# Kernel optimization log

Hardware: AMD Instinct MI355X
Metric: run time of the kernel (lower is better)

## Reference

```python
import jax, jax.numpy as jnp
import numpy as np

B, H, D, DV, N, M = 1, 8, 64, 64, 2048, 128


def setup_inputs() -> dict:
    key = jax.random.key(0)
    k1, k2, k3, k4 = jax.random.split(key, 4)
    keys = jax.random.normal(k1, (B, H, D, N), dtype=jnp.float32)
    values = jax.random.normal(k2, (B, H, DV, N), dtype=jnp.float32)
    queries = jax.random.normal(k3, (B, H, D, N), dtype=jnp.float32)
    # orthonormal random features: QR of (m, key_dim) gaussian (reduced QR, m >= key_dim)
    raw = np.asarray(jax.random.normal(k4, (M, D), dtype=jnp.float32), dtype=np.float64)
    features = jnp.asarray(np.linalg.qr(raw)[0], dtype=jnp.float32)  # (M, D)
    return {"keys": keys, "values": values, "queries": queries, "features": features}


def reference(keys, values, queries, features):
    b, h, d, n = keys.shape
    dv = values.shape[2]
    m = features.shape[0]
    phi_scale = 1.0 / jnp.sqrt(jnp.asarray(m, keys.dtype))
    # flatten heads into batch, move locations to axis 1: (B*H, N, D)
    k = keys.reshape(b * h, d, n).transpose(0, 2, 1)
    v = values.reshape(b * h, dv, n).transpose(0, 2, 1)
    q = queries.reshape(b * h, d, n).transpose(0, 2, 1)

    def phi(x):  # (BH, N, D) -> (BH, N, M); f=[relu], h(x)=1.0
        return jax.nn.relu(jnp.einsum('bnd,md->bnm', x, features)) * phi_scale

    phi_k = phi(k)
    phi_q = phi(q)
    # causal linear attention: prefix sums of phi_k (x) v outer products
    kv = jnp.cumsum(phi_k[:, :, :, None] * v[:, :, None, :], axis=1)  # (BH, N, M, DV)
    out = jnp.einsum('bnm,bnmv->bnv', phi_q, kv)                      # (BH, N, DV)
    norm = jnp.einsum('bnm,bnm->bn', phi_q, jnp.cumsum(phi_k, axis=1))
    out = out / norm[:, :, None]
    out = out.transpose(0, 2, 1).reshape(b, h, dv, n)
    return out
```

## Files before the change

### kernel.cpp

```cpp
#include <hip/hip_runtime.h>


#define BH 8
#define D 64
#define DV 64
#define NSEQ 2048
#define M 128
#define CHK 64
#define NC (NSEQ / CHK)
#define PHI_SCALE 0.08838834764831845f

typedef unsigned int uint;
typedef unsigned short ushort;
typedef __attribute__((ext_vector_type(8))) short bf16x8;
typedef __attribute__((ext_vector_type(4))) short bf16x4;
typedef __attribute__((ext_vector_type(4))) float f32x4;
#define MFMA16(a, b, c) __builtin_amdgcn_mfma_f32_16x16x32_bf16((a), (b), (c), 0, 0, 0)

__device__ __forceinline__ short f2bf(float x) {
    uint u = __float_as_uint(x);
    u += 0x7fffu + ((u >> 16) & 1u);
    return (short)(u >> 16);
}
__device__ __forceinline__ float bf2f(short b) {
    return __uint_as_float(((uint)(ushort)b) << 16);
}

#define SWZ64(r, c)  ((r) * 64  + ((c) ^ (((r) & 7) << 3)))
#define SWZ128(r, c) ((r) * 128 + ((c) ^ (((r) & 7) << 3)))

__global__ __launch_bounds__(256) void favor_p1(
    const float* __restrict__ keys, const float* __restrict__ values,
    const float* __restrict__ queries, const float* __restrict__ features,
    ushort* __restrict__ St, float* __restrict__ z,
    ushort* __restrict__ pQg, ushort* __restrict__ pKg)
{
    const int bh = blockIdx.x >> 5, c = blockIdx.x & 31, n0 = c * CHK;
    const int tid = threadIdx.x;
    const int lane = tid & 63, wid = tid >> 6, quad = lane >> 4, l16 = lane & 15;

    __shared__ ulong2 smv[4096];
    short* sF    = (short*)smv;
    short* sPKmn = (short*)smv + 8192;
    short* sPQt  = (short*)smv + 16384;
    short* sPKt  = (short*)smv + 24576;

    const float* Kb = keys    + bh * D * NSEQ + n0 + 16 * wid + l16;
    const float* Qb = queries + bh * D * NSEQ + n0 + 16 * wid + l16;
    bf16x8 bK[2], aQ[2], aV[2];
    for (int h = 0; h < 2; ++h)
        for (int j = 0; j < 8; ++j) {
            const int d = 32 * h + 8 * quad + j;
            bK[h][j] = f2bf(Kb[d * NSEQ]);
            aQ[h][j] = f2bf(Qb[d * NSEQ]);
        }
    {
        const float* Vb = values + bh * DV * NSEQ + n0;
        for (int h = 0; h < 2; ++h) {
            const float4* vp = (const float4*)(Vb + (16 * wid + l16) * NSEQ + 32 * h + 8 * quad);
            float4 v0 = vp[0], v1 = vp[1];
            aV[h][0] = f2bf(v0.x); aV[h][1] = f2bf(v0.y);
            aV[h][2] = f2bf(v0.z); aV[h][3] = f2bf(v0.w);
            aV[h][4] = f2bf(v1.x); aV[h][5] = f2bf(v1.y);
            aV[h][6] = f2bf(v1.z); aV[h][7] = f2bf(v1.w);
        }
    }
    for (int k = 0; k < 8; ++k) {
        const int i = tid + 256 * k;
        float4 f = ((const float4*)features)[i];
        const int e = 4 * i, row = e >> 6, col = e & 63;
        bf16x4 bq;
        bq[0] = f2bf(f.x); bq[1] = f2bf(f.y); bq[2] = f2bf(f.z); bq[3] = f2bf(f.w);
        *(bf16x4*)(sF + SWZ64(row, col)) = bq;
    }
    __syncthreads();

    for (int mt = 0; mt < 8; ++mt) {
        f32x4 aMN = {0.f,0.f,0.f,0.f}, aQm = {0.f,0.f,0.f,0.f}, aKm = {0.f,0.f,0.f,0.f};
        for (int h = 0; h < 2; ++h) {
            bf16x8 fF = *(const bf16x8*)(sF + SWZ64(16 * mt + l16, 32 * h + 8 * quad));
            aMN = MFMA16(fF, bK[h], aMN);
            aQm = MFMA16(aQ[h], fF, aQm);
            aKm = MFMA16(bK[h], fF, aKm);
        }
        for (int r = 0; r < 4; ++r) {
            const int mr = 16 * mt + 4 * quad + r;
            sPKmn[SWZ64(mr, 16 * wid + l16)] = f2bf(fmaxf(aMN[r], 0.f) * PHI_SCALE);
            const int nr = 16 * wid + 4 * quad + r;
            sPQt[SWZ128(nr, 16 * mt + l16)] = f2bf(fmaxf(aQm[r], 0.f) * PHI_SCALE);
            sPKt[SWZ128(nr, 16 * mt + l16)] = f2bf(fmaxf(aKm[r], 0.f) * PHI_SCALE);
        }
    }
    __syncthreads();

    if (tid < 128) {
        float s = 0.f;
        for (int k = 0; k < 8; ++k) {
            bf16x8 v8 = *(const bf16x8*)(sPKmn + SWZ64(tid, 8 * k));
            for (int j = 0; j < 8; ++j) s += bf2f(v8[j]);
        }
        z[(bh * NC + c) * M + tid] = s;
    }

    {
        ushort* So = St + (size_t)(bh * NC + c) * (DV * M);
        for (int mt = 0; mt < 8; ++mt) {
            f32x4 acc = {0.f,0.f,0.f,0.f};
            for (int h = 0; h < 2; ++h) {
                bf16x8 bP = *(const bf16x8*)(sPKmn + SWZ64(16 * mt + l16, 32 * h + 8 * quad));
                acc = MFMA16(aV[h], bP, acc);
            }
            for (int r = 0; r < 4; ++r)
                So[(16 * wid + 4 * quad + r) * M + 16 * mt + l16] = (ushort)f2bf(acc[r]);
        }
    }

    {
        ushort* pQc = pQg + (size_t)(bh * NC + c) * 8192;
        ushort* pKc = pKg + (size_t)(bh * NC + c) * 8192;
        const ulong2* sq = (const ulong2*)sPQt;
        const ulong2* sk = (const ulong2*)sPKt;
        for (int i = tid; i < 1024; i += 256) {
            ((ulong2*)pQc)[i] = sq[i];
            ((ulong2*)pKc)[i] = sk[i];
        }
    }
}

__global__ __launch_bounds__(256) void favor_p2k(
    const float* __restrict__ values, const ushort* __restrict__ St,
    const float* __restrict__ z, const ushort* __restrict__ pQg,
    const ushort* __restrict__ pKg, float* __restrict__ out)
{
    const int bh = blockIdx.x >> 5, c = blockIdx.x & 31, n0 = c * CHK;
    const int tid = threadIdx.x;
    const int lane = tid & 63, wid = tid >> 6, quad = lane >> 4, l16 = lane & 15;

    __shared__ ulong2 smv[4144];
    short* sPQt = (short*)smv;
    short* sPKt = (short*)smv + 8192;
    short* sSx  = (short*)smv + 16384;
    short* sV   = (short*)smv + 24576;
    short* sAm  = (short*)smv + 28672;
    float* sNm  = (float*)((char*)smv + 65536);
    float* sZ   = (float*)((char*)smv + 65792);
    float* sOut = (float*)((char*)smv + 32768);

    {
        const ulong2* pQc = (const ulong2*)(pQg + (size_t)(bh * NC + c) * 8192);
        const ulong2* pKc = (const ulong2*)(pKg + (size_t)(bh * NC + c) * 8192);
        ulong2* dq = (ulong2*)sPQt;
        ulong2* dk = (ulong2*)sPKt;
        for (int i = tid; i < 1024; i += 256) {
            dq[i] = pQc[i];
            dk[i] = pKc[i];
        }
    }

    {
        const int v = tid >> 2, cb = (tid & 3) * 16;
        const float4* vp = (const float4*)(values + (bh * DV + v) * NSEQ + n0 + cb);
        float4 f0 = vp[0], f1 = vp[1], f2 = vp[2], f3 = vp[3];
        bf16x8 lo, hi;
        lo[0] = f2bf(f0.x); lo[1] = f2bf(f0.y); lo[2] = f2bf(f0.z); lo[3] = f2bf(f0.w);
        lo[4] = f2bf(f1.x); lo[5] = f2bf(f1.y); lo[6] = f2bf(f1.z); lo[7] = f2bf(f1.w);
        hi[0] = f2bf(f2.x); hi[1] = f2bf(f2.y); hi[2] = f2bf(f2.z); hi[3] = f2bf(f2.w);
        hi[4] = f2bf(f3.x); hi[5] = f2bf(f3.y); hi[6] = f2bf(f3.z); hi[7] = f2bf(f3.w);
        *(bf16x8*)(sV + SWZ64(v, cb))     = lo;
        *(bf16x8*)(sV + SWZ64(v, cb + 8)) = hi;
    }

    if (tid < 128) {
        float s = 0.f;
        const float* zp = z + bh * NC * M + tid;
        #pragma unroll 4
        for (int cc = 0; cc < c; ++cc) s += zp[cc * M];
        sZ[tid] = s;
    }

    {
        float a32[4][8];
        #pragma unroll
        for (int k = 0; k < 4; ++k)
            #pragma unroll
            for (int j = 0; j < 8; ++j) a32[k][j] = 0.f;
        const ushort* Sb = St + (size_t)bh * NC * 8192;
        for (int cc = 0; cc < c; ++cc) {
            const ushort* p = Sb + (size_t)cc * 8192;
            #pragma unroll
            for (int k = 0; k < 4; ++k) {
                bf16x8 v8 = *(const bf16x8*)(p + 8 * (tid + 256 * k));
                #pragma unroll
                for (int j = 0; j < 8; ++j) a32[k][j] += bf2f(v8[j]);
            }
        }
        #pragma unroll
        for (int k = 0; k < 4; ++k) {
            const int e = tid + 256 * k;
            bf16x8 w;
            #pragma unroll
            for (int j = 0; j < 8; ++j) w[j] = f2bf(a32[k][j]);
            *(bf16x8*)(sSx + SWZ128(e >> 4, 8 * (e & 15))) = w;
        }
    }
    __syncthreads();

    f32x4 accO[4], accC[4];
    for (int t = 0; t < 4; ++t) { accO[t] = (f32x4){0.f,0.f,0.f,0.f}; accC[t] = (f32x4){0.f,0.f,0.f,0.f}; }
    for (int mt = 0; mt < 4; ++mt) {
        bf16x8 aP = *(const bf16x8*)(sPQt + SWZ128(16 * wid + l16, 32 * mt + 8 * quad));
        for (int jt = 0; jt < 4; ++jt) {
            bf16x8 bK2 = *(const bf16x8*)(sPKt + SWZ128(16 * jt + l16, 32 * mt + 8 * quad));
            accC[jt] = MFMA16(aP, bK2, accC[jt]);
        }
    }
    float rsum[4] = {0.f, 0.f, 0.f, 0.f};
    for (int jt = 0; jt < 4; ++jt)
        for (int r = 0; r < 4; ++r) {
            const int n = 16 * wid + 4 * quad + r;
            const int j = 16 * jt + l16;
            const float av = (j <= n) ? accC[jt][r] : 0.f;
            rsum[r] += av;
            sAm[SWZ64(n, j)] = f2bf(av);
        }
    for (int r = 0; r < 4; ++r) {
        float s = rsum[r];
        s += __shfl_xor(s, 1); s += __shfl_xor(s, 2);
        s += __shfl_xor(s, 4); s += __shfl_xor(s, 8);
        if (l16 == 0) sNm[16 * wid + 4 * quad + r] = s;
    }
    __syncthreads();

    for (int jh = 0; jh < 2; ++jh) {
        bf16x8 aA = *(const bf16x8*)(sAm + SWZ64(16 * wid + l16, 32 * jh + 8 * quad));
        for (int vt = 0; vt < 4; ++vt) {
            bf16x8 bV = *(const bf16x8*)(sV + SWZ64(16 * vt + l16, 32 * jh + 8 * quad));
            accO[vt] = MFMA16(aA, bV, accO[vt]);
        }
    }
    for (int mt = 0; mt < 4; ++mt) {
        bf16x8 aP = *(const bf16x8*)(sPQt + SWZ128(16 * wid + l16, 32 * mt + 8 * quad));
        for (int vt = 0; vt < 4; ++vt) {
            bf16x8 bS = *(const bf16x8*)(sSx + SWZ128(16 * vt + l16, 32 * mt + 8 * quad));
            accO[vt] = MFMA16(aP, bS, accO[vt]);
        }
    }
    if (tid < 64) {
        float s = 0.f;
        for (int mm = 0; mm < 128; ++mm) {
            const int m = (mm + 2 * tid) & 127;
            s += bf2f(sPQt[SWZ128(tid, m)]) * sZ[m];
        }
        sNm[tid] += s;
    }
    __syncthreads();

    for (int vt = 0; vt < 4; ++vt)
        for (int r = 0; r < 4; ++r) {
            const int n = 16 * wid + 4 * quad + r, v = 16 * vt + l16;
            sOut[n * 65 + v] = accO[vt][r] / sNm[n];
        }
    __syncthreads();
    for (int i = tid; i < 4096; i += 256) {
        const int v = i >> 6, n = i & 63;
        out[(bh * DV + v) * NSEQ + n0 + n] = sOut[n * 65 + v];
    }
}

extern "C" void kernel_launch(void* const* d_in, const int* in_sizes, int n_in,
                              void* d_out, int out_size, void* d_ws, size_t ws_size,
                              hipStream_t stream)
{
    (void)in_sizes; (void)n_in; (void)out_size; (void)ws_size;
    const float* keys     = (const float*)d_in[0];
    const float* values   = (const float*)d_in[1];
    const float* queries  = (const float*)d_in[2];
    const float* features = (const float*)d_in[3];
    float* outp = (float*)d_out;

    char* w = (char*)d_ws;
    ushort* St  = (ushort*)w;
    float*  z   = (float*)(w + (size_t)4 * 1024 * 1024);
    ushort* pQg = (ushort*)(w + (size_t)4 * 1024 * 1024 + 128 * 1024);
    ushort* pKg = (ushort*)(w + (size_t)8 * 1024 * 1024 + 128 * 1024);

    favor_p1<<<dim3(BH * NC), dim3(256), 0, stream>>>(keys, values, queries, features,
                                                      St, z, pQg, pKg);
    favor_p2k<<<dim3(BH * NC), dim3(256), 0, stream>>>(values, St, z, pQg, pKg, outp);
}
```

Measured before the change: 99.33 us.

## Replace per-chunk quadratic prefix summation with a separate exclusive-scan kernel

Adds a middle kernel that turns the per-chunk KV states and key-feature sums in workspace into exclusive prefix sums in place. The final kernel then reads only its own chunk's prefix instead of re-summing all earlier chunks, removing the O(NC^2) global reads. It also spreads the normalizer dot product across all four waves and reads the KV state straight from global memory into the MFMA operands, dropping an LDS staging buffer and shrinking shared memory. The cost is an extra kernel launch and a serial 32-step scan per thread.

```diff
diff --git a/kernel.cpp b/kernel.cpp
--- a/kernel.cpp
+++ b/kernel.cpp
@@ -127,7 +127,35 @@
     }
 }
 
-__global__ __launch_bounds__(256) void favor_p2k(
+__global__ __launch_bounds__(256) void favor_p2(ushort* __restrict__ St,
+                                                float* __restrict__ z)
+{
+    const int gid = blockIdx.x * 256 + threadIdx.x;
+    if (blockIdx.x < 256) {
+        const int bh = gid >> 13, vm = gid & 8191;
+        ushort* p = St + (size_t)bh * NC * 8192 + vm;
+        float vals[NC];
+        #pragma unroll
+        for (int cc = 0; cc < NC; ++cc) vals[cc] = bf2f(p[cc * 8192]);
+        float run = 0.f;
+        #pragma unroll
+        for (int cc = 0; cc < NC; ++cc) { p[cc * 8192] = (ushort)f2bf(run); run += vals[cc]; }
+    } else {
+        const int i = gid - 65536;
+        if (i < BH * M) {
+            const int bh = i >> 7, m = i & 127;
+            float* p = z + bh * NC * M + m;
+            float vals[NC];
+            #pragma unroll
+            for (int cc = 0; cc < NC; ++cc) vals[cc] = p[cc * M];
+            float run = 0.f;
+            #pragma unroll
+            for (int cc = 0; cc < NC; ++cc) { p[cc * M] = run; run += vals[cc]; }
+        }
+    }
+}
+
+__global__ __launch_bounds__(256) void favor_p3(
     const float* __restrict__ values, const ushort* __restrict__ St,
     const float* __restrict__ z, const ushort* __restrict__ pQg,
     const ushort* __restrict__ pKg, float* __restrict__ out)
@@ -136,15 +164,15 @@
     const int tid = threadIdx.x;
     const int lane = tid & 63, wid = tid >> 6, quad = lane >> 4, l16 = lane & 15;
 
-    __shared__ ulong2 smv[4144];
+    __shared__ ulong2 smv[3184];
     short* sPQt = (short*)smv;
     short* sPKt = (short*)smv + 8192;
-    short* sSx  = (short*)smv + 16384;
-    short* sV   = (short*)smv + 24576;
-    short* sAm  = (short*)smv + 28672;
-    float* sNm  = (float*)((char*)smv + 65536);
-    float* sZ   = (float*)((char*)smv + 65792);
-    float* sOut = (float*)((char*)smv + 32768);
+    short* sV   = (short*)smv + 16384;
+    short* sAm  = (short*)smv + 20480;
+    float* sNm  = (float*)((char*)smv + 49152);
+    float* sNmP = (float*)((char*)smv + 49408);
+    float* sZ   = (float*)((char*)smv + 50432);
+    float* sOut = (float*)smv;
 
     {
         const ulong2* pQc = (const ulong2*)(pQg + (size_t)(bh * NC + c) * 8192);
@@ -156,7 +184,6 @@
             dk[i] = pKc[i];
         }
     }
-
     {
         const int v = tid >> 2, cb = (tid & 3) * 16;
         const float4* vp = (const float4*)(values + (bh * DV + v) * NSEQ + n0 + cb);
@@ -169,40 +196,7 @@
         *(bf16x8*)(sV + SWZ64(v, cb))     = lo;
         *(bf16x8*)(sV + SWZ64(v, cb + 8)) = hi;
     }
-
-    if (tid < 128) {
-        float s = 0.f;
-        const float* zp = z + bh * NC * M + tid;
-        #pragma unroll 4
-        for (int cc = 0; cc < c; ++cc) s += zp[cc * M];
-        sZ[tid] = s;
-    }
-
-    {
-        float a32[4][8];
-        #pragma unroll
-        for (int k = 0; k < 4; ++k)
-            #pragma unroll
-            for (int j = 0; j < 8; ++j) a32[k][j] = 0.f;
-        const ushort* Sb = St + (size_t)bh * NC * 8192;
-        for (int cc = 0; cc < c; ++cc) {
-            const ushort* p = Sb + (size_t)cc * 8192;
-            #pragma unroll
-            for (int k = 0; k < 4; ++k) {
-                bf16x8 v8 = *(const bf16x8*)(p + 8 * (tid + 256 * k));
-                #pragma unroll
-                for (int j = 0; j < 8; ++j) a32[k][j] += bf2f(v8[j]);
-            }
-        }
-        #pragma unroll
-        for (int k = 0; k < 4; ++k) {
-            const int e = tid + 256 * k;
-            bf16x8 w;
-            #pragma unroll
-            for (int j = 0; j < 8; ++j) w[j] = f2bf(a32[k][j]);
-            *(bf16x8*)(sSx + SWZ128(e >> 4, 8 * (e & 15))) = w;
-        }
-    }
+    if (tid < 128) sZ[tid] = z[(bh * NC + c) * M + tid];
     __syncthreads();
 
     f32x4 accO[4], accC[4];
@@ -229,6 +223,26 @@
         s += __shfl_xor(s, 4); s += __shfl_xor(s, 8);
         if (l16 == 0) sNm[16 * wid + 4 * quad + r] = s;
     }
+
+    {
+        const ushort* Sb = St + (size_t)(bh * NC + c) * (DV * M);
+        for (int mt = 0; mt < 4; ++mt) {
+            bf16x8 aP = *(const bf16x8*)(sPQt + SWZ128(16 * wid + l16, 32 * mt + 8 * quad));
+            for (int vt = 0; vt < 4; ++vt) {
+                bf16x8 bS = *(const bf16x8*)(Sb + (16 * vt + l16) * M + 32 * mt + 8 * quad);
+                accO[vt] = MFMA16(aP, bS, accO[vt]);
+            }
+        }
+    }
+    {
+        const int n = tid & 63, g = tid >> 6;
+        float s = 0.f;
+        for (int mm = 0; mm < 32; ++mm) {
+            const int m = 32 * g + ((mm + n) & 31);
+            s += bf2f(sPQt[SWZ128(n, m)]) * sZ[m];
+        }
+        sNmP[n * 4 + g] = s;
+    }
     __syncthreads();
 
     for (int jh = 0; jh < 2; ++jh) {
@@ -238,21 +252,8 @@
             accO[vt] = MFMA16(aA, bV, accO[vt]);
         }
     }
-    for (int mt = 0; mt < 4; ++mt) {
-        bf16x8 aP = *(const bf16x8*)(sPQt + SWZ128(16 * wid + l16, 32 * mt + 8 * quad));
-        for (int vt = 0; vt < 4; ++vt) {
-            bf16x8 bS = *(const bf16x8*)(sSx + SWZ128(16 * vt + l16, 32 * mt + 8 * quad));
-            accO[vt] = MFMA16(aP, bS, accO[vt]);
-        }
-    }
-    if (tid < 64) {
-        float s = 0.f;
-        for (int mm = 0; mm < 128; ++mm) {
-            const int m = (mm + 2 * tid) & 127;
-            s += bf2f(sPQt[SWZ128(tid, m)]) * sZ[m];
-        }
-        sNm[tid] += s;
-    }
+    if (tid < 64)
+        sNm[tid] += sNmP[tid * 4] + sNmP[tid * 4 + 1] + sNmP[tid * 4 + 2] + sNmP[tid * 4 + 3];
     __syncthreads();
 
     for (int vt = 0; vt < 4; ++vt)
@@ -286,5 +287,6 @@
 
     favor_p1<<<dim3(BH * NC), dim3(256), 0, stream>>>(keys, values, queries, features,
                                                       St, z, pQg, pKg);
-    favor_p2k<<<dim3(BH * NC), dim3(256), 0, stream>>>(values, St, z, pQg, pKg, outp);
-}
+    favor_p2<<<dim3(260), dim3(256), 0, stream>>>(St, z);
+    favor_p3<<<dim3(BH * NC), dim3(256), 0, stream>>>(values, St, z, pQg, pKg, outp);
+}
```

Result: faster. 89.25 us (-10.1%).
